# Optimization experiments

Hardware: AMD Instinct MI355X
Metric: run time of the kernel (lower is better)

## Reference

```python
import jax, jax.numpy as jnp
import numpy as np

jax.config.update("jax_enable_x64", True)  # int64 keys for lattice hashing

_EPS = float(np.finfo(np.float64).eps)
_SIGMA_SPATIAL = 5.0   # spatial stddev (voxels)
_SIGMA_COLOR = 0.25    # intensity stddev
_BASE = 8192           # per-coordinate key range
_OFF = 4096            # coordinate offset so packed keys are non-negative


def _encode(coords):
    """Pack (..., d) integer lattice coords into a single int64 key."""
    enc = jnp.zeros(coords.shape[:-1], jnp.int64)
    for i in range(coords.shape[-1]):
        enc = enc * _BASE + (coords[..., i].astype(jnp.int64) + _OFF)
    return enc


def _bilateral_features(image):
    """Bilateral features: (z,y,x)/sigma_s and intensity/sigma_c. image: (1,D,H,W)."""
    _, D, H, W = image.shape
    z, y, x = jnp.meshgrid(jnp.arange(D, dtype=jnp.float32),
                           jnp.arange(H, dtype=jnp.float32),
                           jnp.arange(W, dtype=jnp.float32), indexing="ij")
    spatial = jnp.stack([z, y, x], -1) / _SIGMA_SPATIAL            # (D,H,W,3)
    color = (image[0] / _SIGMA_COLOR)[..., None]                   # (D,H,W,1)
    return jnp.concatenate([spatial, color], -1).reshape(-1, 4)    # (N,4)


def _permutohedral(q, feats):
    """Permutohedral-lattice Gaussian filtering (splat -> blur -> slice).
    q: (N,C) float32 values, feats: (N,d) float32 positions. Returns (N,C).
    Global scale of the blur kernel cancels in the final normalization."""
    N, d = feats.shape
    dp1 = d + 1
    # ---- elevate features onto the hyperplane H_d ----
    inv_std = np.sqrt(2.0 / 3.0) * dp1
    scale = jnp.asarray([inv_std / np.sqrt((i + 1) * (i + 2)) for i in range(d)], jnp.float32)
    cf = feats * scale
    elev = [None] * dp1
    sm = jnp.zeros((N,), jnp.float32)
    for i in range(d, 0, -1):
        c = cf[:, i - 1]
        elev[i] = sm - i * c
        sm = sm + c
    elev[0] = sm
    elevated = jnp.stack(elev, axis=1)                             # (N, d+1)
    # ---- closest remainder-0 lattice point ----
    rd = jnp.round(elevated / dp1)
    rem0 = rd * dp1
    sum_rd = jnp.sum(rd, axis=1).astype(jnp.int32)
    # ---- rank of each coordinate (ties broken by index) ----
    diff = elevated - rem0
    di = diff[:, :, None]
    dj = diff[:, None, :]
    jlt = (jnp.arange(dp1)[None, :] < jnp.arange(dp1)[:, None])[None]  # mask[i,j] = j < i
    rank = jnp.sum((dj > di) | ((dj == di) & jlt), axis=2).astype(jnp.int32)
    rank = rank + sum_rd[:, None]
    low, high = rank < 0, rank > d
    rank = rank + jnp.where(low, dp1, 0) - jnp.where(high, dp1, 0)
    rem0 = rem0 + jnp.where(low, float(dp1), 0.0) - jnp.where(high, float(dp1), 0.0)
    # ---- barycentric coordinates inside the enclosing simplex ----
    v = (elevated - rem0) / dp1
    rows = jnp.arange(N)[:, None]
    bary = jnp.zeros((N, d + 2), jnp.float32)
    bary = bary.at[rows, d - rank].add(v)
    bary = bary.at[rows, dp1 - rank].add(-v)
    bary = bary.at[:, 0].add(1.0 + bary[:, dp1])
    bary = bary[:, :dp1]                                           # (N, d+1) weights per remainder
    # ---- integer keys of the d+1 simplex vertices (first d coords suffice) ----
    rem0i = rem0[:, :d].astype(jnp.int32)
    keys = jnp.stack([rem0i + jnp.where(rank[:, :d] < dp1 - r, r, r - dp1).astype(jnp.int32)
                      for r in range(dp1)], axis=1)                # (N, d+1, d)
    enc = _encode(keys).reshape(-1)
    Mpad = N * dp1
    sentinel = _BASE ** d                                          # > any real key; sorts last
    uniq, inv = jnp.unique(enc, return_inverse=True, size=Mpad, fill_value=sentinel)
    inv = inv.reshape(N, dp1)
    # ---- splat ----
    C = q.shape[1]
    vals = jnp.zeros((Mpad, C), jnp.float32).at[inv].add(bary[:, :, None] * q[:, None, :])
    # ---- blur along each of the d+1 lattice directions ----
    coords = jnp.stack([(uniq // (_BASE ** (d - 1 - i))) % _BASE - _OFF for i in range(d)],
                       axis=-1).astype(jnp.int32)                  # (Mpad, d)

    def lookup(c):
        e = _encode(c)
        pos = jnp.clip(jnp.searchsorted(uniq, e), 0, Mpad - 1)
        return pos, uniq[pos] == e

    for j in range(dp1):
        off = jnp.ones((d,), jnp.int32)
        if j < d:
            off = off.at[j].set(-d)
        p1, f1 = lookup(coords + off)
        p2, f2 = lookup(coords - off)
        n1 = jnp.where(f1[:, None], vals[p1], 0.0)
        n2 = jnp.where(f2[:, None], vals[p2], 0.0)
        vals = 0.5 * vals + 0.25 * (n1 + n2)
    # ---- slice ----
    return jnp.sum(bary[:, :, None] * vals[inv], axis=1)           # (N, C)


def setup_inputs():
    key = jax.random.key(0)
    k1, k2 = jax.random.split(key)
    input_ = jax.random.uniform(k1, (4, 96, 96, 96), dtype=jnp.float32)
    image = jax.random.uniform(k2, (1, 96, 96, 96), dtype=jnp.float32)
    return {"input_": input_, "image": image}


def reference(input_, image):
    feats = _bilateral_features(image)
    C, D, H, W = input_.shape
    q = input_.reshape(C, -1).T                                    # (N, C)
    ones = jnp.ones((q.shape[0], 1), jnp.float32)                  # fused normalization pass
    filt = _permutohedral(jnp.concatenate([q, ones], axis=1), feats)
    out = filt[:, :C] / (filt[:, C:] + _EPS)                       # == permuto(q) * 1/(permuto(1)+eps)
    return out.T.reshape(C, D, H, W)
```

## Files before the change

kernel.cpp:

```cpp
#include <hip/hip_runtime.h>
#include <hip/hip_fp16.h>
#include <stdint.h>

#define NPTS (96*96*96)
#define NP5  (NPTS*5)

#define GD1 33
#define GD2 29
#define GD3 25
#define GO0 5
#define GO1 16
#define GO2 18
#define GO3 19
#define GS3 5
#define GS2 (GD3*GS3)
#define GS1 (GD2*GS2)
#define GS0 (GD1*GS1)
#define GCELLS (31*GS0)
#define GCELLS1 (GCELLS+1)
#define GSSUM (GS0+GS1+GS2+GS3)

#define LHSR 512

struct LatPt { int cell[5]; float w[5]; };
struct V5 { float s0, s1, s2, s3, w; };


#define LATTICE_MATH(n)                                                        \
  int x = n % 96, y = (n / 96) % 96, z = n / (96 * 96);                        \
  float cf[4];                                                                 \
  cf[0] = ((float)z / 5.0f) * 2.8867513459481287f;                             \
  cf[1] = ((float)y / 5.0f) * 1.6666666666666667f;                             \
  cf[2] = ((float)x / 5.0f) * 1.1785113019775793f;                             \
  cf[3] = (imgv / 0.25f) * 0.9128709291752769f;                                \
  float elev[5];                                                               \
  float sm = 0.f;                                                              \
  _Pragma("unroll")                                                            \
  for (int i = 4; i >= 1; --i){ float c = cf[i-1]; elev[i] = sm - (float)i * c; sm += c; } \
  elev[0] = sm;                                                                \
  float rem0[5]; float sumrd_f = 0.f;                                          \
  _Pragma("unroll")                                                            \
  for (int i = 0; i < 5; i++){ float rd = rintf(elev[i] / 5.0f); rem0[i] = rd * 5.0f; sumrd_f += rd; } \
  int sum_rd = (int)sumrd_f;                                                   \
  float diff[5];                                                               \
  _Pragma("unroll")                                                            \
  for (int i = 0; i < 5; i++) diff[i] = elev[i] - rem0[i];                     \
  int rank[5];                                                                 \
  _Pragma("unroll")                                                            \
  for (int i = 0; i < 5; i++){                                                 \
    int r = 0;                                                                 \
    _Pragma("unroll")                                                          \
    for (int j = 0; j < 5; j++){                                               \
      r += (diff[j] > diff[i] || (diff[j] == diff[i] && j < i)) ? 1 : 0;       \
    }                                                                          \
    rank[i] = r + sum_rd;                                                      \
  }                                                                            \
  _Pragma("unroll")                                                            \
  for (int i = 0; i < 5; i++){                                                 \
    if (rank[i] < 0)      { rank[i] += 5; rem0[i] += 5.0f; }                   \
    else if (rank[i] > 4) { rank[i] -= 5; rem0[i] -= 5.0f; }                   \
  }                                                                            \
  float b[6] = {0.f,0.f,0.f,0.f,0.f,0.f};                                      \
  _Pragma("unroll")                                                            \
  for (int i = 0; i < 5; i++){                                                 \
    float v = (elev[i] - rem0[i]) / 5.0f;                                      \
    b[4 - rank[i]] += v;                                                       \
    b[5 - rank[i]] -= v;                                                       \
  }                                                                            \
  b[0] += 1.0f + b[5];                                                         \
  int rem0i[4];                                                                \
  _Pragma("unroll")                                                            \
  for (int i = 0; i < 4; i++) rem0i[i] = (int)rem0[i];

__device__ __forceinline__ LatPt lat_compute(int n, float imgv)
{
  LATTICE_MATH(n)
  LatPt p;
  #pragma unroll
  for (int r = 0; r < 5; r++){
    int q0 = (rem0i[0] / 5) - (rank[0] < 5 - r ? 0 : 1) + GO0;
    int q1 = (rem0i[1] / 5) - (rank[1] < 5 - r ? 0 : 1) + GO1;
    int q2 = (rem0i[2] / 5) - (rank[2] < 5 - r ? 0 : 1) + GO2;
    int q3 = (rem0i[3] / 5) - (rank[3] < 5 - r ? 0 : 1) + GO3;
    int cell = (((q0 * GD1 + q1) * GD2 + q2) * GD3 + q3) * 5 + r;
    if ((unsigned)cell >= (unsigned)GCELLS) cell = GCELLS;
    p.cell[r] = cell;
    p.w[r] = b[r];
  }
  return p;
}

__global__ void k_build_hyb(const float* __restrict__ image,
                            const float* __restrict__ input_,
                            int* __restrict__ head,
                            int4* __restrict__ nodes)
{
  __shared__ int   ls_cells[5 * LHSR];
  __shared__ short ls_next[5 * 256];
  __shared__ float ls_w[5 * 256];
  __shared__ float ls_q[256 * 4];
  __shared__ short ls_slot[1280];
  __shared__ int   ls_cnt;

  int tid = threadIdx.x;
  #pragma unroll
  for (int i = 0; i < (5 * LHSR) / 256; i++)
    ls_cells[tid + 256 * i] = -1;
  if (tid == 0) ls_cnt = 0;
  __syncthreads();

  int n = blockIdx.x * 256 + tid;
  float q0 = input_[n], q1 = input_[NPTS + n], q2 = input_[2 * NPTS + n], q3 = input_[3 * NPTS + n];
  *reinterpret_cast<float4*>(&ls_q[tid * 4]) = make_float4(q0, q1, q2, q3);
  LatPt P = lat_compute(n, image[n]);

  #pragma unroll
  for (int r = 0; r < 5; r++){
    int cell = P.cell[r];
    if (cell < GCELLS){
      int pos = cell / 5;
      unsigned int h = ((unsigned int)pos * 2654435761u) >> 23;
      int base = r * LHSR;
      int me = (pos << 9) | tid;
      while (true){
        int cur = ls_cells[base + h];
        if (cur == -1){
          cur = atomicCAS(&ls_cells[base + h], -1, me);
          if (cur == -1){
            ls_next[r * 256 + tid] = 511;
            int li = atomicAdd(&ls_cnt, 1);
            ls_slot[li] = (short)(base + h);
            break;
          }
        }
        if ((cur >> 9) == pos){
          int old = atomicExch(&ls_cells[base + h], me);
          ls_next[r * 256 + tid] = (short)(old & 511);
          break;
        }
        h = (h + 1) & (LHSR - 1);
      }
      ls_w[r * 256 + tid] = P.w[r];
    }
  }
  __syncthreads();

  int cnt = ls_cnt;
  int blockBase = blockIdx.x * 1280;
  for (int i = tid; i < cnt; i += 256){
    int slot = ls_slot[i];
    int word = ls_cells[slot];
    int r = slot >> 9;
    int pos = word >> 9;
    int cell = pos * 5 + r;
    float s0 = 0.f, s1 = 0.f, s2 = 0.f, s3 = 0.f, s4 = 0.f;
    int e = word & 511;
    while (e < 256){
      int en = ls_next[r * 256 + e];
      float w = ls_w[r * 256 + e];
      float4 q = *reinterpret_cast<const float4*>(&ls_q[e * 4]);
      s0 += w * q.x; s1 += w * q.y; s2 += w * q.z; s3 += w * q.w; s4 += w;
      e = en;
    }
    int node = blockBase + i;
    int old = atomicExch(&head[cell], node);
    __half2 h01 = __floats2half2_rn(s0, s1);
    __half2 h23 = __floats2half2_rn(s2, s3);
    int4 raw;
    raw.x = old;
    raw.y = *reinterpret_cast<int*>(&h01);
    raw.z = *reinterpret_cast<int*>(&h23);
    raw.w = __float_as_int(s4);
    nodes[node] = raw;
  }
}

__global__ void k_gather_agg(const int* __restrict__ head,
                             const int4* __restrict__ nodes,
                             int3* __restrict__ vals,
                             unsigned int* __restrict__ bitmap)
{
  int c = blockIdx.x * blockDim.x + threadIdx.x;
  int e = -1;
  if (c < GCELLS1) e = head[c];
  bool occ = (e >= 0);
  unsigned long long mask = __ballot(occ);
  int lane = threadIdx.x & 63;
  if (lane == 0)       bitmap[c >> 5] = (unsigned int)(mask & 0xffffffffu);
  else if (lane == 32) bitmap[c >> 5] = (unsigned int)(mask >> 32);
  if (c >= GCELLS1) return;

  float s0 = 0.f, s1 = 0.f, s2 = 0.f, s3 = 0.f, s4 = 0.f;
  while (e >= 0){
    int4 raw = nodes[e];
    __half2 h01 = *reinterpret_cast<__half2*>(&raw.y);
    __half2 h23 = *reinterpret_cast<__half2*>(&raw.z);
    float2 f01 = __half22float2(h01);
    float2 f23 = __half22float2(h23);
    s0 += f01.x; s1 += f01.y; s2 += f23.x; s3 += f23.y;
    s4 += __int_as_float(raw.w);
    e = raw.x;
  }
  __half2 o01 = __floats2half2_rn(s0, s1);
  __half2 o23 = __floats2half2_rn(s2, s3);
  int3 rec;
  rec.x = *reinterpret_cast<int*>(&o01);
  rec.y = *reinterpret_cast<int*>(&o23);
  rec.z = __float_as_int(s4);
  vals[c] = rec;
}

__device__ __forceinline__ V5 ublur(const unsigned int* __restrict__ bitmap,
                                    const int3* __restrict__ vin,
                                    int d, int dPa, int dPb, int dMa, int dMb)
{
  V5 u = {0.f, 0.f, 0.f, 0.f, 0.f};
  unsigned int wd = bitmap[d >> 5];
  if (!((wd >> (d & 31)) & 1u)) return u;
  int rd = d % 5;
  int p1 = d + (rd == 4 ? dPb : dPa);
  int p2 = d + (rd == 0 ? dMb : dMa);
  int3 a  = vin[d];
  int3 b1 = vin[p1];
  int3 b2 = vin[p2];
  float2 a01 = __half22float2(*reinterpret_cast<__half2*>(&a.x));
  float2 a23 = __half22float2(*reinterpret_cast<__half2*>(&a.y));
  float2 m01 = __half22float2(*reinterpret_cast<__half2*>(&b1.x));
  float2 m23 = __half22float2(*reinterpret_cast<__half2*>(&b1.y));
  float2 n01 = __half22float2(*reinterpret_cast<__half2*>(&b2.x));
  float2 n23 = __half22float2(*reinterpret_cast<__half2*>(&b2.y));
  u.s0 = 0.5f * a01.x + 0.25f * (m01.x + n01.x);
  u.s1 = 0.5f * a01.y + 0.25f * (m01.y + n01.y);
  u.s2 = 0.5f * a23.x + 0.25f * (m23.x + n23.x);
  u.s3 = 0.5f * a23.y + 0.25f * (m23.y + n23.y);
  u.w  = 0.5f * __int_as_float(a.z) + 0.25f * (__int_as_float(b1.z) + __int_as_float(b2.z));
  return u;
}

__global__ void k_blur2_d(const unsigned int* __restrict__ bitmap,
                          const int3* __restrict__ vin,
                          int3* __restrict__ vout,
                          int dPaA, int dPbA, int dMaA, int dMbA,
                          int dPaB, int dPbB, int dMaB, int dMbB, int zfill)
{
  int c = blockIdx.x * blockDim.x + threadIdx.x;
  if (c >= GCELLS) return;
  unsigned int w = bitmap[c >> 5];
  if (!((w >> (c & 31)) & 1u)){
    if (zfill){
      int3 zero; zero.x = 0; zero.y = 0; zero.z = 0;
      vout[c] = zero;
    }
    return;
  }
  int r = c % 5;
  int q1 = c + (r == 4 ? dPbB : dPaB);
  int q2 = c + (r == 0 ? dMbB : dMaB);

  V5 uc = ublur(bitmap, vin, c,  dPaA, dPbA, dMaA, dMbA);
  V5 u1 = ublur(bitmap, vin, q1, dPaA, dPbA, dMaA, dMbA);
  V5 u2 = ublur(bitmap, vin, q2, dPaA, dPbA, dMaA, dMbA);

  float o0 = 0.5f * uc.s0 + 0.25f * (u1.s0 + u2.s0);
  float o1 = 0.5f * uc.s1 + 0.25f * (u1.s1 + u2.s1);
  float o2 = 0.5f * uc.s2 + 0.25f * (u1.s2 + u2.s2);
  float o3 = 0.5f * uc.s3 + 0.25f * (u1.s3 + u2.s3);
  float ow = 0.5f * uc.w  + 0.25f * (u1.w  + u2.w);

  __half2 o01 = __floats2half2_rn(o0, o1);
  __half2 o23 = __floats2half2_rn(o2, o3);
  int3 rec;
  rec.x = *reinterpret_cast<int*>(&o01);
  rec.y = *reinterpret_cast<int*>(&o23);
  rec.z = __float_as_int(ow);
  vout[c] = rec;
}

__global__ void k_blur_d(const unsigned int* __restrict__ bitmap,
                         const int3* __restrict__ vin,
                         int3* __restrict__ vout,
                         int dPa, int dPb, int dMa, int dMb, int zfill)
{
  int c = blockIdx.x * blockDim.x + threadIdx.x;
  if (c >= GCELLS) return;
  unsigned int w = bitmap[c >> 5];
  if (!((w >> (c & 31)) & 1u)){
    if (zfill){
      int3 zero; zero.x = 0; zero.y = 0; zero.z = 0;
      vout[c] = zero;
    }
    return;
  }
  V5 u = ublur(bitmap, vin, c, dPa, dPb, dMa, dMb);
  __half2 o01 = __floats2half2_rn(u.s0, u.s1);
  __half2 o23 = __floats2half2_rn(u.s2, u.s3);
  int3 rec;
  rec.x = *reinterpret_cast<int*>(&o01);
  rec.y = *reinterpret_cast<int*>(&o23);
  rec.z = __float_as_int(u.w);
  vout[c] = rec;
}

__global__ void k_slice_d(const float* __restrict__ image,
                          const int3* __restrict__ vals,
                          float* __restrict__ out)
{
  int n = blockIdx.x * blockDim.x + threadIdx.x;
  if (n >= NPTS) return;
  LatPt P = lat_compute(n, image[n]);

  float s0 = 0.f, s1 = 0.f, s2 = 0.f, s3 = 0.f, s4 = 0.f;
  #pragma unroll
  for (int r = 0; r < 5; r++){
    float w = P.w[r];
    int3 rec = vals[P.cell[r]];
    float2 f01 = __half22float2(*reinterpret_cast<__half2*>(&rec.x));
    float2 f23 = __half22float2(*reinterpret_cast<__half2*>(&rec.y));
    s0 += w * f01.x; s1 += w * f01.y; s2 += w * f23.x; s3 += w * f23.y;
    s4 += w * __int_as_float(rec.z);
  }
  float denom = s4 + 2.2204460492503131e-16f;
  out[n]            = s0 / denom;
  out[NPTS + n]     = s1 / denom;
  out[2 * NPTS + n] = s2 / denom;
  out[3 * NPTS + n] = s3 / denom;
}


extern "C" void kernel_launch(void* const* d_in, const int* in_sizes, int n_in,
                              void* d_out, int out_size, void* d_ws, size_t ws_size,
                              hipStream_t stream)
{
  const float* input_ = (const float*)d_in[0];
  const float* image  = (const float*)d_in[1];
  float* out = (float*)d_out;
  char* ws = (char*)d_ws;

  const int NB = (NPTS + 255) / 256;
  const int CB = (GCELLS1 + 255) / 256;
  const size_t BMWORDS = (size_t)CB * 8;
  const int Sj[5] = { GS0, GS1, GS2, GS3, 0 };
  int dPa[5], dPb[5], dMa[5], dMb[5];
  for (int j = 0; j < 5; j++){
    dPa[j] = 1 - Sj[j];
    dPb[j] = GSSUM - Sj[j] - 4;
    dMa[j] = Sj[j] - 1;
    dMb[j] = Sj[j] - GSSUM + 4;
  }

  size_t o = 0;
  size_t off_bm   = o; o += BMWORDS * 4;              o = (o + 255) & ~(size_t)255;
  size_t off_dead = o;
  size_t off_head = o; o += (size_t)GCELLS1 * 4;      o = (o + 255) & ~(size_t)255;
  size_t off_node = o; o += (size_t)NP5 * 16;         o = (o + 255) & ~(size_t)255;
  size_t dead_end = o;
  size_t off_vA   = o; o += (size_t)GCELLS1 * 12;
  size_t vB_need  = (size_t)GCELLS1 * 12;
  size_t off_vB   = off_dead;
  if (dead_end - off_dead < vB_need || o > ws_size){
    off_vB = (o + 255) & ~(size_t)255;
  }

  unsigned int* bitmap = (unsigned int*)(ws + off_bm);
  int*          head   = (int*)(ws + off_head);
  int4*         nodes  = (int4*)(ws + off_node);
  int3*         valsA  = (int3*)(ws + off_vA);
  int3*         valsB  = (int3*)(ws + off_vB);

  hipMemsetAsync(head, 0xFF, (size_t)GCELLS1 * 4, stream);

  k_build_hyb<<<NB, 256, 0, stream>>>(image, input_, head, nodes);
  k_gather_agg<<<CB, 256, 0, stream>>>(head, nodes, valsA, bitmap);

  k_blur2_d<<<CB, 256, 0, stream>>>(bitmap, valsA, valsB,
                                    dPa[0], dPb[0], dMa[0], dMb[0],
                                    dPa[1], dPb[1], dMa[1], dMb[1], 1);
  k_blur2_d<<<CB, 256, 0, stream>>>(bitmap, valsB, valsA,
                                    dPa[2], dPb[2], dMa[2], dMb[2],
                                    dPa[3], dPb[3], dMa[3], dMb[3], 0);
  k_blur_d<<<CB, 256, 0, stream>>>(bitmap, valsA, valsB,
                                   dPa[4], dPb[4], dMa[4], dMb[4], 0);

  k_slice_d<<<NB, 256, 0, stream>>>(image, valsB, out);
}
```

Measured before the change: 175.1 us.

## Fuse last three blur directions into one kernel and dual-walk splat chains

The separate blur kernels for directions 3 and 4 are merged with direction 2 into one kernel that recomputes the intermediate blurs from neighbours on the fly. This removes one launch and one full read/write pass over the lattice value array. In exchange each output cell does 27 neighbour gathers instead of 3, which is extra redundant memory traffic and arithmetic. Separately, the splat aggregation loop now lets each thread walk two linked-list chains at once to raise instruction-level parallelism on the dependent shared-memory loads.

```diff
diff --git a/kernel.cpp b/kernel.cpp
--- a/kernel.cpp
+++ b/kernel.cpp
@@ -147,31 +147,58 @@
 
   int cnt = ls_cnt;
   int blockBase = blockIdx.x * 1280;
-  for (int i = tid; i < cnt; i += 256){
-    int slot = ls_slot[i];
-    int word = ls_cells[slot];
-    int r = slot >> 9;
-    int pos = word >> 9;
-    int cell = pos * 5 + r;
-    float s0 = 0.f, s1 = 0.f, s2 = 0.f, s3 = 0.f, s4 = 0.f;
-    int e = word & 511;
-    while (e < 256){
-      int en = ls_next[r * 256 + e];
-      float w = ls_w[r * 256 + e];
-      float4 q = *reinterpret_cast<const float4*>(&ls_q[e * 4]);
-      s0 += w * q.x; s1 += w * q.y; s2 += w * q.z; s3 += w * q.w; s4 += w;
-      e = en;
-    }
-    int node = blockBase + i;
-    int old = atomicExch(&head[cell], node);
-    __half2 h01 = __floats2half2_rn(s0, s1);
-    __half2 h23 = __floats2half2_rn(s2, s3);
-    int4 raw;
-    raw.x = old;
-    raw.y = *reinterpret_cast<int*>(&h01);
-    raw.z = *reinterpret_cast<int*>(&h23);
-    raw.w = __float_as_int(s4);
-    nodes[node] = raw;
+  for (int base = 0; base < cnt; base += 512){
+    int i1 = base + tid;
+    int i2 = i1 + 256;
+    bool v1 = (i1 < cnt), v2 = (i2 < cnt);
+    int slot1 = 0, slot2 = 0, word1 = 0, word2 = 0;
+    int e1 = 256, e2 = 256, r1 = 0, r2 = 0;
+    if (v1){ slot1 = ls_slot[i1]; word1 = ls_cells[slot1]; e1 = word1 & 511; r1 = slot1 >> 9; }
+    if (v2){ slot2 = ls_slot[i2]; word2 = ls_cells[slot2]; e2 = word2 & 511; r2 = slot2 >> 9; }
+    float s10 = 0.f, s11 = 0.f, s12 = 0.f, s13 = 0.f, s14 = 0.f;
+    float s20 = 0.f, s21 = 0.f, s22 = 0.f, s23 = 0.f, s24 = 0.f;
+    while (e1 < 256 || e2 < 256){
+      if (e1 < 256){
+        int en = ls_next[r1 * 256 + e1];
+        float w = ls_w[r1 * 256 + e1];
+        float4 q = *reinterpret_cast<const float4*>(&ls_q[e1 * 4]);
+        s10 += w * q.x; s11 += w * q.y; s12 += w * q.z; s13 += w * q.w; s14 += w;
+        e1 = en;
+      }
+      if (e2 < 256){
+        int en = ls_next[r2 * 256 + e2];
+        float w = ls_w[r2 * 256 + e2];
+        float4 q = *reinterpret_cast<const float4*>(&ls_q[e2 * 4]);
+        s20 += w * q.x; s21 += w * q.y; s22 += w * q.z; s23 += w * q.w; s24 += w;
+        e2 = en;
+      }
+    }
+    if (v1){
+      int cell = (word1 >> 9) * 5 + r1;
+      int node = blockBase + i1;
+      int old = atomicExch(&head[cell], node);
+      __half2 h01 = __floats2half2_rn(s10, s11);
+      __half2 h23 = __floats2half2_rn(s12, s13);
+      int4 raw;
+      raw.x = old;
+      raw.y = *reinterpret_cast<int*>(&h01);
+      raw.z = *reinterpret_cast<int*>(&h23);
+      raw.w = __float_as_int(s14);
+      nodes[node] = raw;
+    }
+    if (v2){
+      int cell = (word2 >> 9) * 5 + r2;
+      int node = blockBase + i2;
+      int old = atomicExch(&head[cell], node);
+      __half2 h01 = __floats2half2_rn(s20, s21);
+      __half2 h23 = __floats2half2_rn(s22, s23);
+      int4 raw;
+      raw.x = old;
+      raw.y = *reinterpret_cast<int*>(&h01);
+      raw.z = *reinterpret_cast<int*>(&h23);
+      raw.w = __float_as_int(s24);
+      nodes[node] = raw;
+    }
   }
 }
 
@@ -237,6 +264,28 @@
   return u;
 }
 
+__device__ __forceinline__ V5 ublur2(const unsigned int* __restrict__ bitmap,
+                                     const int3* __restrict__ vin, int d,
+                                     int dPaA, int dPbA, int dMaA, int dMbA,
+                                     int dPaB, int dPbB, int dMaB, int dMbB)
+{
+  V5 o = {0.f, 0.f, 0.f, 0.f, 0.f};
+  unsigned int wd = bitmap[d >> 5];
+  if (!((wd >> (d & 31)) & 1u)) return o;
+  int r = d % 5;
+  int q1 = d + (r == 4 ? dPbB : dPaB);
+  int q2 = d + (r == 0 ? dMbB : dMaB);
+  V5 uc = ublur(bitmap, vin, d,  dPaA, dPbA, dMaA, dMbA);
+  V5 u1 = ublur(bitmap, vin, q1, dPaA, dPbA, dMaA, dMbA);
+  V5 u2 = ublur(bitmap, vin, q2, dPaA, dPbA, dMaA, dMbA);
+  o.s0 = 0.5f * uc.s0 + 0.25f * (u1.s0 + u2.s0);
+  o.s1 = 0.5f * uc.s1 + 0.25f * (u1.s1 + u2.s1);
+  o.s2 = 0.5f * uc.s2 + 0.25f * (u1.s2 + u2.s2);
+  o.s3 = 0.5f * uc.s3 + 0.25f * (u1.s3 + u2.s3);
+  o.w  = 0.5f * uc.w  + 0.25f * (u1.w  + u2.w);
+  return o;
+}
+
 __global__ void k_blur2_d(const unsigned int* __restrict__ bitmap,
                           const int3* __restrict__ vin,
                           int3* __restrict__ vout,
@@ -253,33 +302,22 @@
     }
     return;
   }
-  int r = c % 5;
-  int q1 = c + (r == 4 ? dPbB : dPaB);
-  int q2 = c + (r == 0 ? dMbB : dMaB);
-
-  V5 uc = ublur(bitmap, vin, c,  dPaA, dPbA, dMaA, dMbA);
-  V5 u1 = ublur(bitmap, vin, q1, dPaA, dPbA, dMaA, dMbA);
-  V5 u2 = ublur(bitmap, vin, q2, dPaA, dPbA, dMaA, dMbA);
-
-  float o0 = 0.5f * uc.s0 + 0.25f * (u1.s0 + u2.s0);
-  float o1 = 0.5f * uc.s1 + 0.25f * (u1.s1 + u2.s1);
-  float o2 = 0.5f * uc.s2 + 0.25f * (u1.s2 + u2.s2);
-  float o3 = 0.5f * uc.s3 + 0.25f * (u1.s3 + u2.s3);
-  float ow = 0.5f * uc.w  + 0.25f * (u1.w  + u2.w);
-
-  __half2 o01 = __floats2half2_rn(o0, o1);
-  __half2 o23 = __floats2half2_rn(o2, o3);
+  V5 o = ublur2(bitmap, vin, c, dPaA, dPbA, dMaA, dMbA, dPaB, dPbB, dMaB, dMbB);
+  __half2 o01 = __floats2half2_rn(o.s0, o.s1);
+  __half2 o23 = __floats2half2_rn(o.s2, o.s3);
   int3 rec;
   rec.x = *reinterpret_cast<int*>(&o01);
   rec.y = *reinterpret_cast<int*>(&o23);
-  rec.z = __float_as_int(ow);
+  rec.z = __float_as_int(o.w);
   vout[c] = rec;
 }
 
-__global__ void k_blur_d(const unsigned int* __restrict__ bitmap,
-                         const int3* __restrict__ vin,
-                         int3* __restrict__ vout,
-                         int dPa, int dPb, int dMa, int dMb, int zfill)
+__global__ void k_blur3_d(const unsigned int* __restrict__ bitmap,
+                          const int3* __restrict__ vin,
+                          int3* __restrict__ vout,
+                          int dPaA, int dPbA, int dMaA, int dMbA,
+                          int dPaB, int dPbB, int dMaB, int dMbB,
+                          int dPaC, int dPbC, int dMaC, int dMbC, int zfill)
 {
   int c = blockIdx.x * blockDim.x + threadIdx.x;
   if (c >= GCELLS) return;
@@ -291,13 +329,26 @@
     }
     return;
   }
-  V5 u = ublur(bitmap, vin, c, dPa, dPb, dMa, dMb);
-  __half2 o01 = __floats2half2_rn(u.s0, u.s1);
-  __half2 o23 = __floats2half2_rn(u.s2, u.s3);
+  int r = c % 5;
+  int p1 = c + (r == 4 ? dPbC : dPaC);
+  int p2 = c + (r == 0 ? dMbC : dMaC);
+
+  V5 uc = ublur2(bitmap, vin, c,  dPaA, dPbA, dMaA, dMbA, dPaB, dPbB, dMaB, dMbB);
+  V5 u1 = ublur2(bitmap, vin, p1, dPaA, dPbA, dMaA, dMbA, dPaB, dPbB, dMaB, dMbB);
+  V5 u2 = ublur2(bitmap, vin, p2, dPaA, dPbA, dMaA, dMbA, dPaB, dPbB, dMaB, dMbB);
+
+  float o0 = 0.5f * uc.s0 + 0.25f * (u1.s0 + u2.s0);
+  float o1 = 0.5f * uc.s1 + 0.25f * (u1.s1 + u2.s1);
+  float o2 = 0.5f * uc.s2 + 0.25f * (u1.s2 + u2.s2);
+  float o3 = 0.5f * uc.s3 + 0.25f * (u1.s3 + u2.s3);
+  float ow = 0.5f * uc.w  + 0.25f * (u1.w  + u2.w);
+
+  __half2 o01 = __floats2half2_rn(o0, o1);
+  __half2 o23 = __floats2half2_rn(o2, o3);
   int3 rec;
   rec.x = *reinterpret_cast<int*>(&o01);
   rec.y = *reinterpret_cast<int*>(&o23);
-  rec.z = __float_as_int(u.w);
+  rec.z = __float_as_int(ow);
   vout[c] = rec;
 }
 
@@ -375,11 +426,10 @@
   k_blur2_d<<<CB, 256, 0, stream>>>(bitmap, valsA, valsB,
                                     dPa[0], dPb[0], dMa[0], dMb[0],
                                     dPa[1], dPb[1], dMa[1], dMb[1], 1);
-  k_blur2_d<<<CB, 256, 0, stream>>>(bitmap, valsB, valsA,
+  k_blur3_d<<<CB, 256, 0, stream>>>(bitmap, valsB, valsA,
                                     dPa[2], dPb[2], dMa[2], dMb[2],
-                                    dPa[3], dPb[3], dMa[3], dMb[3], 0);
-  k_blur_d<<<CB, 256, 0, stream>>>(bitmap, valsA, valsB,
-                                   dPa[4], dPb[4], dMa[4], dMb[4], 0);
-
-  k_slice_d<<<NB, 256, 0, stream>>>(image, valsB, out);
-}
+                                    dPa[3], dPb[3], dMa[3], dMb[3],
+                                    dPa[4], dPb[4], dMa[4], dMb[4], 0);
+
+  k_slice_d<<<NB, 256, 0, stream>>>(image, valsA, out);
+}
```

Measured after the change: 175.1 us. No clear change (-0.0%).

## Fuse last three blur directions into one kernel and batch hash probes

Applied to the files above, without the earlier changes.

Replaces the second two-direction blur and the final single-direction blur with one three-direction kernel. It recomputes the inner two-direction stencil for each of the three outer neighbours, which removes one launch and one intermediate write/read of the lattice values. In exchange each output cell gathers 27 cells instead of the previous 12 loads across two passes. The splat's hash insertion is also restructured: the first probe for all five vertices is issued together before the linear-probe loops, to overlap LDS latency.

```diff
diff --git a/kernel.cpp b/kernel.cpp
--- a/kernel.cpp
+++ b/kernel.cpp
@@ -114,34 +114,59 @@
   *reinterpret_cast<float4*>(&ls_q[tid * 4]) = make_float4(q0, q1, q2, q3);
   LatPt P = lat_compute(n, image[n]);
 
+  int hh[5], me[5], basev[5], stat[5], curv[5];
   #pragma unroll
   for (int r = 0; r < 5; r++){
     int cell = P.cell[r];
     if (cell < GCELLS){
       int pos = cell / 5;
-      unsigned int h = ((unsigned int)pos * 2654435761u) >> 23;
-      int base = r * LHSR;
-      int me = (pos << 9) | tid;
-      while (true){
-        int cur = ls_cells[base + h];
-        if (cur == -1){
-          cur = atomicCAS(&ls_cells[base + h], -1, me);
-          if (cur == -1){
-            ls_next[r * 256 + tid] = 511;
-            int li = atomicAdd(&ls_cnt, 1);
-            ls_slot[li] = (short)(base + h);
-            break;
-          }
-        }
-        if ((cur >> 9) == pos){
-          int old = atomicExch(&ls_cells[base + h], me);
-          ls_next[r * 256 + tid] = (short)(old & 511);
+      hh[r]    = (int)(((unsigned)pos * 2654435761u) >> 23);
+      basev[r] = r * LHSR;
+      me[r]    = (pos << 9) | tid;
+      stat[r]  = 0;
+    } else {
+      stat[r] = 3;
+    }
+  }
+  #pragma unroll
+  for (int r = 0; r < 5; r++)
+    if (stat[r] == 0) curv[r] = ls_cells[basev[r] + hh[r]];
+
+  #pragma unroll
+  for (int r = 0; r < 5; r++){
+    if (stat[r] == 3) continue;
+    int pos = me[r] >> 9;
+    int h = hh[r];
+    int cur = curv[r];
+    while (true){
+      if (cur == -1){
+        int prev = atomicCAS(&ls_cells[basev[r] + h], -1, me[r]);
+        if (prev == -1){
+          ls_next[r * 256 + tid] = 511;
+          int li = atomicAdd(&ls_cnt, 1);
+          ls_slot[li] = (short)(basev[r] + h);
+          stat[r] = 2; hh[r] = h;
           break;
         }
-        h = (h + 1) & (LHSR - 1);
+        cur = prev;
+        continue;
       }
-      ls_w[r * 256 + tid] = P.w[r];
-    }
+      if ((cur >> 9) == pos){
+        stat[r] = 1; hh[r] = h;
+        break;
+      }
+      h = (h + 1) & (LHSR - 1);
+      cur = ls_cells[basev[r] + h];
+    }
+  }
+
+  #pragma unroll
+  for (int r = 0; r < 5; r++){
+    if (stat[r] == 1){
+      int old = atomicExch(&ls_cells[basev[r] + hh[r]], me[r]);
+      ls_next[r * 256 + tid] = (short)(old & 511);
+    }
+    if (stat[r] != 3) ls_w[r * 256 + tid] = P.w[r];
   }
   __syncthreads();
 
@@ -237,6 +262,28 @@
   return u;
 }
 
+__device__ __forceinline__ V5 ublur2(const unsigned int* __restrict__ bitmap,
+                                     const int3* __restrict__ vin, int d,
+                                     int dPaA, int dPbA, int dMaA, int dMbA,
+                                     int dPaB, int dPbB, int dMaB, int dMbB)
+{
+  V5 o = {0.f, 0.f, 0.f, 0.f, 0.f};
+  unsigned int wd = bitmap[d >> 5];
+  if (!((wd >> (d & 31)) & 1u)) return o;
+  int r = d % 5;
+  int q1 = d + (r == 4 ? dPbB : dPaB);
+  int q2 = d + (r == 0 ? dMbB : dMaB);
+  V5 uc = ublur(bitmap, vin, d,  dPaA, dPbA, dMaA, dMbA);
+  V5 u1 = ublur(bitmap, vin, q1, dPaA, dPbA, dMaA, dMbA);
+  V5 u2 = ublur(bitmap, vin, q2, dPaA, dPbA, dMaA, dMbA);
+  o.s0 = 0.5f * uc.s0 + 0.25f * (u1.s0 + u2.s0);
+  o.s1 = 0.5f * uc.s1 + 0.25f * (u1.s1 + u2.s1);
+  o.s2 = 0.5f * uc.s2 + 0.25f * (u1.s2 + u2.s2);
+  o.s3 = 0.5f * uc.s3 + 0.25f * (u1.s3 + u2.s3);
+  o.w  = 0.5f * uc.w  + 0.25f * (u1.w  + u2.w);
+  return o;
+}
+
 __global__ void k_blur2_d(const unsigned int* __restrict__ bitmap,
                           const int3* __restrict__ vin,
                           int3* __restrict__ vout,
@@ -253,33 +300,22 @@
     }
     return;
   }
-  int r = c % 5;
-  int q1 = c + (r == 4 ? dPbB : dPaB);
-  int q2 = c + (r == 0 ? dMbB : dMaB);
-
-  V5 uc = ublur(bitmap, vin, c,  dPaA, dPbA, dMaA, dMbA);
-  V5 u1 = ublur(bitmap, vin, q1, dPaA, dPbA, dMaA, dMbA);
-  V5 u2 = ublur(bitmap, vin, q2, dPaA, dPbA, dMaA, dMbA);
-
-  float o0 = 0.5f * uc.s0 + 0.25f * (u1.s0 + u2.s0);
-  float o1 = 0.5f * uc.s1 + 0.25f * (u1.s1 + u2.s1);
-  float o2 = 0.5f * uc.s2 + 0.25f * (u1.s2 + u2.s2);
-  float o3 = 0.5f * uc.s3 + 0.25f * (u1.s3 + u2.s3);
-  float ow = 0.5f * uc.w  + 0.25f * (u1.w  + u2.w);
-
-  __half2 o01 = __floats2half2_rn(o0, o1);
-  __half2 o23 = __floats2half2_rn(o2, o3);
+  V5 o = ublur2(bitmap, vin, c, dPaA, dPbA, dMaA, dMbA, dPaB, dPbB, dMaB, dMbB);
+  __half2 o01 = __floats2half2_rn(o.s0, o.s1);
+  __half2 o23 = __floats2half2_rn(o.s2, o.s3);
   int3 rec;
   rec.x = *reinterpret_cast<int*>(&o01);
   rec.y = *reinterpret_cast<int*>(&o23);
-  rec.z = __float_as_int(ow);
+  rec.z = __float_as_int(o.w);
   vout[c] = rec;
 }
 
-__global__ void k_blur_d(const unsigned int* __restrict__ bitmap,
-                         const int3* __restrict__ vin,
-                         int3* __restrict__ vout,
-                         int dPa, int dPb, int dMa, int dMb, int zfill)
+__global__ void k_blur3_d(const unsigned int* __restrict__ bitmap,
+                          const int3* __restrict__ vin,
+                          int3* __restrict__ vout,
+                          int dPaA, int dPbA, int dMaA, int dMbA,
+                          int dPaB, int dPbB, int dMaB, int dMbB,
+                          int dPaC, int dPbC, int dMaC, int dMbC, int zfill)
 {
   int c = blockIdx.x * blockDim.x + threadIdx.x;
   if (c >= GCELLS) return;
@@ -291,13 +327,26 @@
     }
     return;
   }
-  V5 u = ublur(bitmap, vin, c, dPa, dPb, dMa, dMb);
-  __half2 o01 = __floats2half2_rn(u.s0, u.s1);
-  __half2 o23 = __floats2half2_rn(u.s2, u.s3);
+  int r = c % 5;
+  int p1 = c + (r == 4 ? dPbC : dPaC);
+  int p2 = c + (r == 0 ? dMbC : dMaC);
+
+  V5 uc = ublur2(bitmap, vin, c,  dPaA, dPbA, dMaA, dMbA, dPaB, dPbB, dMaB, dMbB);
+  V5 u1 = ublur2(bitmap, vin, p1, dPaA, dPbA, dMaA, dMbA, dPaB, dPbB, dMaB, dMbB);
+  V5 u2 = ublur2(bitmap, vin, p2, dPaA, dPbA, dMaA, dMbA, dPaB, dPbB, dMaB, dMbB);
+
+  float o0 = 0.5f * uc.s0 + 0.25f * (u1.s0 + u2.s0);
+  float o1 = 0.5f * uc.s1 + 0.25f * (u1.s1 + u2.s1);
+  float o2 = 0.5f * uc.s2 + 0.25f * (u1.s2 + u2.s2);
+  float o3 = 0.5f * uc.s3 + 0.25f * (u1.s3 + u2.s3);
+  float ow = 0.5f * uc.w  + 0.25f * (u1.w  + u2.w);
+
+  __half2 o01 = __floats2half2_rn(o0, o1);
+  __half2 o23 = __floats2half2_rn(o2, o3);
   int3 rec;
   rec.x = *reinterpret_cast<int*>(&o01);
   rec.y = *reinterpret_cast<int*>(&o23);
-  rec.z = __float_as_int(u.w);
+  rec.z = __float_as_int(ow);
   vout[c] = rec;
 }
 
@@ -375,11 +424,10 @@
   k_blur2_d<<<CB, 256, 0, stream>>>(bitmap, valsA, valsB,
                                     dPa[0], dPb[0], dMa[0], dMb[0],
                                     dPa[1], dPb[1], dMa[1], dMb[1], 1);
-  k_blur2_d<<<CB, 256, 0, stream>>>(bitmap, valsB, valsA,
+  k_blur3_d<<<CB, 256, 0, stream>>>(bitmap, valsB, valsA,
                                     dPa[2], dPb[2], dMa[2], dMb[2],
-                                    dPa[3], dPb[3], dMa[3], dMb[3], 0);
-  k_blur_d<<<CB, 256, 0, stream>>>(bitmap, valsA, valsB,
-                                   dPa[4], dPb[4], dMa[4], dMb[4], 0);
-
-  k_slice_d<<<NB, 256, 0, stream>>>(image, valsB, out);
-}
+                                    dPa[3], dPb[3], dMa[3], dMb[3],
+                                    dPa[4], dPb[4], dMa[4], dMb[4], 0);
+
+  k_slice_d<<<NB, 256, 0, stream>>>(image, valsA, out);
+}
```

Measured after the change: 177.7 us. No clear change (+1.5%).
